# Optimization experiments

Hardware: AMD Instinct MI355X
Metric: run time of the kernel (lower is better)

Reference implementation:

```python
import jax, jax.numpy as jnp
import numpy as np

B, L, H, E, M = 8, 1024, 1024, 2048, 2048  # batch, seq, hidden_dim, expanded_dim, max_seq_length


def setup_inputs() -> dict:
    key = jax.random.key(0)
    ks = jax.random.split(key, 10)
    n = lambda k, shape, s=0.02: jax.random.normal(k, shape, jnp.float32) * s
    return {
        'x': jax.random.normal(ks[0], (B, L, H), jnp.float32),
        'ln1_w': jnp.ones((H,), jnp.float32), 'ln1_b': jnp.zeros((H,), jnp.float32),
        'ln2_w': jnp.ones((E,), jnp.float32), 'ln2_b': jnp.zeros((E,), jnp.float32),
        'w_qkv': n(ks[1], (3 * E, H)), 'b_qkv': jnp.zeros((3 * E,), jnp.float32),
        'w_out': n(ks[2], (H, E)), 'b_out': jnp.zeros((H,), jnp.float32),
        'rel_pos': n(ks[3], (2 * M - 1, H)),
        'w_beta': n(ks[4], (E, 2 * H)), 'b_beta': jnp.zeros((E,), jnp.float32),
        'w1': n(ks[5], (4 * H, H)), 'b1': jnp.zeros((4 * H,), jnp.float32),
        'w2': n(ks[6], (H, 4 * H)), 'b2': jnp.zeros((H,), jnp.float32),
        'conv_w': n(ks[7], (E, 1, 3), 0.3),  # depthwise conv1d weight [C,1,K]
        'attn_scale': jnp.ones((1,), jnp.float32),
    }


def _ln(x, w, b):
    m = jnp.mean(x, -1, keepdims=True)
    v = jnp.mean((x - m) ** 2, -1, keepdims=True)
    return (x - m) / jnp.sqrt(v + 1e-5) * w + b


def _normalize(x):
    # F.normalize(x, dim=-1): x / max(||x||_2, 1e-12)
    return x / jnp.maximum(jnp.linalg.norm(x, axis=-1, keepdims=True), 1e-12)


def _dwconv(z, w):
    # z: [B,L,E]; depthwise conv1d k=3, pad=1, no bias (groups=E)
    y = jax.lax.conv_general_dilated(
        z.transpose(0, 2, 1), w, window_strides=(1,), padding=((1, 1),),
        feature_group_count=w.shape[0], dimension_numbers=('NCH', 'OIH', 'NCH'))
    return y.transpose(0, 2, 1)


def reference(x, ln1_w, ln1_b, ln2_w, ln2_b, w_qkv, b_qkv, w_out, b_out,
              rel_pos, w_beta, b_beta, w1, b1, w2, b2, conv_w, attn_scale):
    Lx = x.shape[1]
    h = _ln(x, ln1_w, ln1_b)
    qkv = h @ w_qkv.T + b_qkv
    q, k, v = jnp.split(qkv, 3, axis=-1)  # each [B,L,E]
    q = jax.nn.silu(q)
    k = jax.nn.silu(k)
    v = jax.nn.gelu(v, approximate=False)
    # interdependent normalize-mix (k uses the updated q)
    q = _normalize(q) + 0.1 * k
    k = _normalize(k) + 0.1 * q
    q = _dwconv(q, conv_w)
    k = _dwconv(k, conv_w)
    v = _dwconv(v, conv_w)
    # position-conditioned beta gate
    pos_embed = rel_pos[:Lx]  # [L,H]
    pos_info = jnp.einsum('blh,mh->blm', h, pos_embed).mean(-1, keepdims=True)  # [B,L,1]
    comb = jnp.concatenate([h, jnp.broadcast_to(pos_info, h.shape)], axis=-1)  # [B,L,2H]
    beta = jax.nn.sigmoid(comb @ w_beta.T + b_beta) * 0.9 + 0.1  # [B,L,E]
    # delta-rule: state starts at zeros so v_old = state @ k^T = 0 exactly
    v_new = beta * v  # beta*v + (1-beta)*0
    state = jnp.einsum('ble,blf->bef', v_new, k)  # v_new^T @ k : [B,E,E]
    out = jnp.einsum('ble,bfe->blf', q, state) * attn_scale  # q @ state^T
    out = _ln(out, ln2_w, ln2_b) @ w_out.T + b_out
    x = x + out
    h2 = _ln(x, ln1_w, ln1_b)  # norm1 is reused pre-MLP
    mlp = jax.nn.gelu(h2 @ w1.T + b1, approximate=False) @ w2.T + b2
    return x + mlp
```

## Files before the change

kernel.cpp:

```cpp
#include <hip/hip_runtime.h>
#include <hip/hip_bf16.h>
#include <math.h>

using bf16 = __hip_bfloat16;
typedef __attribute__((ext_vector_type(8))) short bf16x8;
typedef __attribute__((ext_vector_type(4))) float f32x4;

#define DEVI __device__ __forceinline__

DEVI float b2f(bf16 v) { return __bfloat162float(v); }
DEVI bf16 f2b(float v) { return __float2bfloat16(v); }
DEVI float geluf(float x) { return 0.5f * x * (1.0f + erff(x * 0.70710678118654752f)); }
DEVI float siluf(float x) { return x / (1.0f + expf(-x)); }

DEVI void load_lds16(const bf16* g, bf16* l) {
  __builtin_amdgcn_global_load_lds(
      (const __attribute__((address_space(1))) void*)g,
      (__attribute__((address_space(3))) void*)l, 16, 0, 0);
}

__global__ __launch_bounds__(256) void cast_kernel(const float* __restrict__ in,
                                                   bf16* __restrict__ out, int n4) {
  int i = blockIdx.x * 256 + threadIdx.x;
  if (i >= n4) return;
  float4 v = reinterpret_cast<const float4*>(in)[i];
  bf16 o[4] = { f2b(v.x), f2b(v.y), f2b(v.z), f2b(v.w) };
  reinterpret_cast<uint2*>(out)[i] = *reinterpret_cast<uint2*>(o);
}

__global__ __launch_bounds__(256) void prep_kernel(const float* __restrict__ rel,
                                                   float* __restrict__ pm,
                                                   const float* __restrict__ wb,
                                                   float* __restrict__ wb2s) {
  const int b = blockIdx.x;
  if (b < 4) {
    int h = b * 256 + threadIdx.x;
    float s = 0.f;
    for (int m = 0; m < 1024; ++m) s += rel[m * 1024 + h];
    pm[h] = s * (1.0f / 1024.0f);
  } else {
    int e = (b - 4) * 4 + (threadIdx.x >> 6);
    int lane = threadIdx.x & 63;
    float s = 0.f;
    for (int j = lane; j < 1024; j += 64) s += wb[(long)e * 2048 + 1024 + j];
#pragma unroll
    for (int off = 32; off > 0; off >>= 1) s += __shfl_down(s, off);
    if (lane == 0) wb2s[e] = s;
  }
}

__global__ __launch_bounds__(256) void convw_pack_kernel(const float* __restrict__ cw,
                                                         bf16* __restrict__ wpl) {
  int e = blockIdx.x * 256 + threadIdx.x;
  wpl[e]        = f2b(cw[e * 3]);
  wpl[2048 + e] = f2b(cw[e * 3 + 1]);
  wpl[4096 + e] = f2b(cw[e * 3 + 2]);
}

template<bool POS>
__global__ __launch_bounds__(256) void ln1024_kernel(
    const float* __restrict__ x, const float* __restrict__ w, const float* __restrict__ b,
    bf16* __restrict__ out, const float* __restrict__ pmean, float* __restrict__ pos) {
  __shared__ float red[12];
  long row = blockIdx.x;
  int t = threadIdx.x, lane = t & 63, wid = t >> 6;
  float4 xv = reinterpret_cast<const float4*>(x + row * 1024)[t];
  float s = xv.x + xv.y + xv.z + xv.w;
  float ss = xv.x * xv.x + xv.y * xv.y + xv.z * xv.z + xv.w * xv.w;
#pragma unroll
  for (int off = 32; off > 0; off >>= 1) { s += __shfl_down(s, off); ss += __shfl_down(ss, off); }
  if (lane == 0) { red[wid] = s; red[4 + wid] = ss; }
  __syncthreads();
  s = red[0] + red[1] + red[2] + red[3];
  ss = red[4] + red[5] + red[6] + red[7];
  float mean = s * (1.0f / 1024.0f);
  float rstd = rsqrtf(ss * (1.0f / 1024.0f) - mean * mean + 1e-5f);
  float4 wv = reinterpret_cast<const float4*>(w)[t];
  float4 bv = reinterpret_cast<const float4*>(b)[t];
  float h0 = (xv.x - mean) * rstd * wv.x + bv.x;
  float h1 = (xv.y - mean) * rstd * wv.y + bv.y;
  float h2 = (xv.z - mean) * rstd * wv.z + bv.z;
  float h3 = (xv.w - mean) * rstd * wv.w + bv.w;
  bf16 o[4] = { f2b(h0), f2b(h1), f2b(h2), f2b(h3) };
  reinterpret_cast<uint2*>(out + row * 1024)[t] = *reinterpret_cast<uint2*>(o);
  if (POS) {
    float4 pv = reinterpret_cast<const float4*>(pmean)[t];
    float d = h0 * pv.x + h1 * pv.y + h2 * pv.z + h3 * pv.w;
#pragma unroll
    for (int off = 32; off > 0; off >>= 1) d += __shfl_down(d, off);
    if (lane == 0) red[8 + wid] = d;
    __syncthreads();
    if (t == 0) pos[row] = red[8] + red[9] + red[10] + red[11];
  }
}

__global__ __launch_bounds__(256) void ln1024b_kernel(
    const bf16* __restrict__ x, const float* __restrict__ w, const float* __restrict__ b,
    bf16* __restrict__ out) {
  __shared__ float red[8];
  long row = blockIdx.x;
  int t = threadIdx.x, lane = t & 63, wid = t >> 6;
  bf16 tv[4];
  *reinterpret_cast<uint2*>(tv) = reinterpret_cast<const uint2*>(x + row * 1024)[t];
  float v[4], s = 0.f, ss = 0.f;
#pragma unroll
  for (int j = 0; j < 4; ++j) { v[j] = b2f(tv[j]); s += v[j]; ss += v[j] * v[j]; }
#pragma unroll
  for (int off = 32; off > 0; off >>= 1) { s += __shfl_down(s, off); ss += __shfl_down(ss, off); }
  if (lane == 0) { red[wid] = s; red[4 + wid] = ss; }
  __syncthreads();
  s = red[0] + red[1] + red[2] + red[3];
  ss = red[4] + red[5] + red[6] + red[7];
  float mean = s * (1.0f / 1024.0f);
  float rstd = rsqrtf(ss * (1.0f / 1024.0f) - mean * mean + 1e-5f);
  float4 wv = reinterpret_cast<const float4*>(w)[t];
  float4 bv = reinterpret_cast<const float4*>(b)[t];
  bf16 o[4];
  o[0] = f2b((v[0] - mean) * rstd * wv.x + bv.x);
  o[1] = f2b((v[1] - mean) * rstd * wv.y + bv.y);
  o[2] = f2b((v[2] - mean) * rstd * wv.z + bv.z);
  o[3] = f2b((v[3] - mean) * rstd * wv.w + bv.w);
  reinterpret_cast<uint2*>(out + row * 1024)[t] = *reinterpret_cast<uint2*>(o);
}

__global__ __launch_bounds__(256) void ln2048_bf16_kernel(
    const bf16* __restrict__ in, const float* __restrict__ w, const float* __restrict__ b,
    bf16* __restrict__ out) {
  __shared__ float red[8];
  long row = blockIdx.x;
  int t = threadIdx.x, lane = t & 63, wid = t >> 6;
  bf16 tv[8];
  *reinterpret_cast<int4*>(tv) = reinterpret_cast<const int4*>(in + row * 2048)[t];
  float v[8], s = 0.f, ss = 0.f;
#pragma unroll
  for (int j = 0; j < 8; ++j) { v[j] = b2f(tv[j]); s += v[j]; ss += v[j] * v[j]; }
#pragma unroll
  for (int off = 32; off > 0; off >>= 1) { s += __shfl_down(s, off); ss += __shfl_down(ss, off); }
  if (lane == 0) { red[wid] = s; red[4 + wid] = ss; }
  __syncthreads();
  s = red[0] + red[1] + red[2] + red[3];
  ss = red[4] + red[5] + red[6] + red[7];
  float mean = s * (1.0f / 2048.0f);
  float rstd = rsqrtf(ss * (1.0f / 2048.0f) - mean * mean + 1e-5f);
  int base = t * 8;
  bf16 o[8];
#pragma unroll
  for (int j = 0; j < 8; ++j) o[j] = f2b((v[j] - mean) * rstd * w[base + j] + b[base + j]);
  reinterpret_cast<int4*>(out + row * 2048)[t] = *reinterpret_cast<int4*>(o);
}

__global__ __launch_bounds__(256) void act_norm_kernel(
    bf16* __restrict__ qp, bf16* __restrict__ kp, bf16* __restrict__ vp) {
  __shared__ float red[8];
  long row = blockIdx.x;
  int t = threadIdx.x, lane = t & 63, wid = t >> 6;
  long ob = row * 2048 + t * 8;
  bf16 tq[8], tk[8], tv[8];
  *reinterpret_cast<int4*>(tq) = *reinterpret_cast<const int4*>(qp + ob);
  *reinterpret_cast<int4*>(tk) = *reinterpret_cast<const int4*>(kp + ob);
  *reinterpret_cast<int4*>(tv) = *reinterpret_cast<const int4*>(vp + ob);
  float qs[8], ks[8];
  float sq = 0.f, sk = 0.f;
#pragma unroll
  for (int j = 0; j < 8; ++j) {
    float q = b2f(tq[j]); qs[j] = siluf(q); sq += qs[j] * qs[j];
    float k = b2f(tk[j]); ks[j] = siluf(k); sk += ks[j] * ks[j];
  }
#pragma unroll
  for (int off = 32; off > 0; off >>= 1) { sq += __shfl_down(sq, off); sk += __shfl_down(sk, off); }
  if (lane == 0) { red[wid] = sq; red[4 + wid] = sk; }
  __syncthreads();
  sq = red[0] + red[1] + red[2] + red[3];
  sk = red[4] + red[5] + red[6] + red[7];
  float rq = 1.0f / fmaxf(sqrtf(sq), 1e-12f);
  float rk = 1.0f / fmaxf(sqrtf(sk), 1e-12f);
  bf16 oq[8], ok[8], ov[8];
#pragma unroll
  for (int j = 0; j < 8; ++j) {
    float qn = qs[j] * rq + 0.1f * ks[j];
    float kn = ks[j] * rk + 0.1f * qn;
    oq[j] = f2b(qn); ok[j] = f2b(kn);
    ov[j] = f2b(geluf(b2f(tv[j])));
  }
  *reinterpret_cast<int4*>(qp + ob) = *reinterpret_cast<int4*>(oq);
  *reinterpret_cast<int4*>(kp + ob) = *reinterpret_cast<int4*>(ok);
  *reinterpret_cast<int4*>(vp + ob) = *reinterpret_cast<int4*>(ov);
}

__global__ __launch_bounds__(256) void dwconv2_kernel(
    const bf16* __restrict__ q_in, bf16* __restrict__ q_out,
    const bf16* __restrict__ v_in, bf16* __restrict__ v_out,
    const bf16* __restrict__ wpl) {
  const bf16* in = blockIdx.y ? v_in : q_in;
  bf16* out = blockIdx.y ? v_out : q_out;
  const int t = threadIdx.x;
  const int e0 = t * 8;
  const long bl = blockIdx.x;
  const int l = (int)(bl & 1023);
  const bf16* mid = in + (bl * 2048 + e0);
  bf16 tm[8], tp[8], tn[8], w0[8], w1[8], w2[8];
  *reinterpret_cast<int4*>(tm) = *reinterpret_cast<const int4*>(mid);
  if (l > 0)    *reinterpret_cast<int4*>(tp) = *reinterpret_cast<const int4*>(mid - 2048);
  if (l < 1023) *reinterpret_cast<int4*>(tn) = *reinterpret_cast<const int4*>(mid + 2048);
  *reinterpret_cast<int4*>(w0) = *reinterpret_cast<const int4*>(&wpl[e0]);
  *reinterpret_cast<int4*>(w1) = *reinterpret_cast<const int4*>(&wpl[2048 + e0]);
  *reinterpret_cast<int4*>(w2) = *reinterpret_cast<const int4*>(&wpl[4096 + e0]);
  bf16 o[8];
#pragma unroll
  for (int j = 0; j < 8; ++j) {
    float a = b2f(w1[j]) * b2f(tm[j]);
    if (l > 0) a += b2f(w0[j]) * b2f(tp[j]);
    if (l < 1023) a += b2f(w2[j]) * b2f(tn[j]);
    o[j] = f2b(a);
  }
  *reinterpret_cast<int4*>(out + (bl * 2048 + e0)) = *reinterpret_cast<int4*>(o);
}

__global__ __launch_bounds__(256) void transpose2f_kernel(
    const bf16* __restrict__ in1, bf16* __restrict__ out1,
    const bf16* __restrict__ in2, bf16* __restrict__ out2,
    const bf16* __restrict__ wpl) {
  const int zz = blockIdx.z;
  const bool isk = (zz < 8);
  const bf16* in = isk ? in1 : in2;
  bf16* out = isk ? out1 : out2;
  const long base = (long)(zz & 7) * 2097152;
  const int r0 = blockIdx.y * 64 + ((threadIdx.x & 63) >> 3) * 8;
  const int c0 = blockIdx.x * 256 + (threadIdx.x >> 6) * 64 + (threadIdx.x & 7) * 8;
  bf16 vv[8][8];
  if (isk) {
    bf16 raw[10][8];
#pragma unroll
    for (int j = 0; j < 10; ++j) {
      int r = r0 + j - 1;
      if (r >= 0 && r < 1024)
        *reinterpret_cast<int4*>(raw[j]) =
            *reinterpret_cast<const int4*>(&in[base + (long)r * 2048 + c0]);
      else {
#pragma unroll
        for (int i = 0; i < 8; ++i) raw[j][i] = f2b(0.f);
      }
    }
    bf16 w0[8], w1[8], w2[8];
    *reinterpret_cast<int4*>(w0) = *reinterpret_cast<const int4*>(&wpl[c0]);
    *reinterpret_cast<int4*>(w1) = *reinterpret_cast<const int4*>(&wpl[2048 + c0]);
    *reinterpret_cast<int4*>(w2) = *reinterpret_cast<const int4*>(&wpl[4096 + c0]);
#pragma unroll
    for (int j = 0; j < 8; ++j)
#pragma unroll
      for (int i = 0; i < 8; ++i)
        vv[j][i] = f2b(b2f(w0[i]) * b2f(raw[j][i]) + b2f(w1[i]) * b2f(raw[j + 1][i]) +
                       b2f(w2[i]) * b2f(raw[j + 2][i]));
  } else {
#pragma unroll
    for (int j = 0; j < 8; ++j)
      *reinterpret_cast<int4*>(vv[j]) =
          *reinterpret_cast<const int4*>(&in[base + (long)(r0 + j) * 2048 + c0]);
  }
#pragma unroll
  for (int i = 0; i < 8; ++i) {
    bf16 w[8];
#pragma unroll
    for (int j = 0; j < 8; ++j) w[j] = vv[j][i];
    *reinterpret_cast<int4*>(&out[base + (long)(c0 + i) * 1024 + r0]) =
        *reinterpret_cast<int4*>(w);
  }
}

enum { EPI_QKV = 0, EPI_BETA = 1, EPI_BF16 = 2, EPI_SCALE = 3, EPI_RES_F32 = 4, EPI_GELU = 5 };

#define MF(d, a, b) d = __builtin_amdgcn_mfma_f32_16x16x32_bf16(a, b, d, 0, 0, 0)
#define RD_A(S, MR, KK) \
  (*reinterpret_cast<const bf16x8*>(&smem[(S)*16384 + wm*8192 + ((MR)*16 + r16)*64 + ((((KK)*32) + kq8) ^ swz)]))
#define RD_B(S, NR, KK) \
  (*reinterpret_cast<const bf16x8*>(&smem[32768 + (S)*16384 + (wn>>1)*8192 + ((wn&1)*64 + (NR)*16 + r16)*64 + ((((KK)*32) + kq8) ^ swz)]))
#define STAGE_A1(S, H, Q, KT) \
  load_lds16(Abase + (long)((H)*128 + (Q)*64) * lda + (long)(KT)*64, \
             &smem[(S)*16384 + (H)*8192 + (Q)*4096 + wid*512])
#define STAGE_B1(S, H, Q, KT) \
  load_lds16(Bbase + (long)((H)*128 + (Q)*64) * ldb + (long)(KT)*64, \
             &smem[32768 + (S)*16384 + (H)*8192 + (Q)*4096 + wid*512])
#define STAGE_AH(S, H, KT) { STAGE_A1(S, H, 0, KT); STAGE_A1(S, H, 1, KT); }
#define STAGE_BH(S, H, KT) { STAGE_B1(S, H, 0, KT); STAGE_B1(S, H, 1, KT); }
#define BAR_A __builtin_amdgcn_s_barrier()
#define LGKM0 { asm volatile("s_waitcnt lgkmcnt(0)" ::: "memory"); __builtin_amdgcn_sched_barrier(0); }
#define VWAIT(LST) { if (LST) { asm volatile("s_waitcnt vmcnt(0)" ::: "memory"); } \
                     else     { asm volatile("s_waitcnt vmcnt(6)" ::: "memory"); } \
                     __builtin_amdgcn_sched_barrier(0); }

#define KTILE(S, ST1, ST2, ST3, ST4, W4) { \
  bf16x8 aL[4][2], aH[4][2], bL[2][2], bH[2][2]; \
  _Pragma("unroll") for (int m_ = 0; m_ < 4; ++m_) { aL[m_][0] = RD_A(S, m_, 0); aL[m_][1] = RD_A(S, m_, 1); } \
  _Pragma("unroll") for (int n_ = 0; n_ < 2; ++n_) { bL[n_][0] = RD_B(S, n_, 0); bL[n_][1] = RD_B(S, n_, 1); } \
  ST1; BAR_A; LGKM0; \
  __builtin_amdgcn_s_setprio(1); \
  _Pragma("unroll") for (int m_ = 0; m_ < 4; ++m_) _Pragma("unroll") for (int n_ = 0; n_ < 2; ++n_) { \
    MF(acc[m_][n_], aL[m_][0], bL[n_][0]); MF(acc[m_][n_], aL[m_][1], bL[n_][1]); } \
  __builtin_amdgcn_s_setprio(0); __builtin_amdgcn_s_barrier(); \
  _Pragma("unroll") for (int n_ = 0; n_ < 2; ++n_) { bH[n_][0] = RD_B(S, n_ + 2, 0); bH[n_][1] = RD_B(S, n_ + 2, 1); } \
  ST2; BAR_A; LGKM0; \
  __builtin_amdgcn_s_setprio(1); \
  _Pragma("unroll") for (int m_ = 0; m_ < 4; ++m_) _Pragma("unroll") for (int n_ = 0; n_ < 2; ++n_) { \
    MF(acc[m_][n_ + 2], aL[m_][0], bH[n_][0]); MF(acc[m_][n_ + 2], aL[m_][1], bH[n_][1]); } \
  __builtin_amdgcn_s_setprio(0); __builtin_amdgcn_s_barrier(); \
  _Pragma("unroll") for (int m_ = 0; m_ < 4; ++m_) { aH[m_][0] = RD_A(S, m_ + 4, 0); aH[m_][1] = RD_A(S, m_ + 4, 1); } \
  ST3; BAR_A; LGKM0; \
  __builtin_amdgcn_s_setprio(1); \
  _Pragma("unroll") for (int m_ = 0; m_ < 4; ++m_) _Pragma("unroll") for (int n_ = 0; n_ < 2; ++n_) { \
    MF(acc[m_ + 4][n_], aH[m_][0], bL[n_][0]); MF(acc[m_ + 4][n_], aH[m_][1], bL[n_][1]); } \
  __builtin_amdgcn_s_setprio(0); __builtin_amdgcn_s_barrier(); \
  ST4; W4; BAR_A; LGKM0; \
  __builtin_amdgcn_s_setprio(1); \
  _Pragma("unroll") for (int m_ = 0; m_ < 4; ++m_) _Pragma("unroll") for (int n_ = 0; n_ < 2; ++n_) { \
    MF(acc[m_ + 4][n_ + 2], aH[m_][0], bH[n_][0]); MF(acc[m_ + 4][n_ + 2], aH[m_][1], bH[n_][1]); } \
  __builtin_amdgcn_s_setprio(0); __builtin_amdgcn_s_barrier(); \
}

template<int EPI>
__global__ __launch_bounds__(512) void gemm256_kernel(
    const bf16* __restrict__ A, int lda, long sA,
    const bf16* __restrict__ B, int ldb, long sB,
    void* __restrict__ Cv, int ldc, long sC, int K,
    const float* __restrict__ bias, const float* __restrict__ aux_row,
    const float* __restrict__ aux_col, const bf16* __restrict__ vconv,
    const float* __restrict__ resid, const float* __restrict__ scale_ptr,
    bf16* __restrict__ p2, bf16* __restrict__ p3) {
  __shared__ bf16 smem[65536];
  const int bz = blockIdx.z;
  A += (long)bz * sA;
  B += (long)bz * sB;
  const int m0 = blockIdx.y * 256, n0 = blockIdx.x * 256;
  const int t = threadIdx.x, lane = t & 63, wid = t >> 6;
  const int wm = wid >> 2, wn = wid & 3;
  const int r16 = lane & 15, kq8 = (lane >> 4) * 8;
  const int swz = (r16 & 7) << 3;
  const int lrow = lane >> 3;
  const int cswz = ((lane & 7) ^ lrow) * 8;
  const bf16* Abase = A + (long)(m0 + wid * 8 + lrow) * lda + cswz;
  const bf16* Bbase = B + (long)(n0 + wid * 8 + lrow) * ldb + cswz;
  f32x4 acc[8][4] = {};
  const int NT = K >> 6, NIT = NT >> 1;
  STAGE_AH(0, 0, 0); STAGE_AH(0, 1, 0); STAGE_BH(0, 0, 0); STAGE_BH(0, 1, 0);
  STAGE_BH(1, 0, 1); STAGE_BH(1, 1, 1); STAGE_AH(1, 0, 1);
  asm volatile("s_waitcnt vmcnt(6)" ::: "memory");
  __builtin_amdgcn_sched_barrier(0);
  __builtin_amdgcn_s_barrier();
  for (int i = 0; i < NIT; ++i) {
    const int tb = 2 * i;
    const bool lst = (i == NIT - 1);
    KTILE(0,
      { STAGE_AH(1, 1, tb + 1); },
      { },
      { if (!lst) { STAGE_BH(0, 0, tb + 2); STAGE_BH(0, 1, tb + 2); } },
      { if (!lst) { STAGE_AH(0, 0, tb + 2); } },
      VWAIT(lst));
    KTILE(1,
      { if (!lst) { STAGE_AH(0, 1, tb + 2); } },
      { },
      { if (!lst) { STAGE_BH(1, 0, tb + 3); STAGE_BH(1, 1, tb + 3); } },
      { if (!lst) { STAGE_AH(1, 0, tb + 3); } },
      VWAIT(lst));
  }
  float scl = 1.0f;
  if (EPI == EPI_SCALE) scl = scale_ptr[0];
  const int rb = (lane >> 4) * 4;
#pragma unroll
  for (int mr = 0; mr < 8; ++mr) {
#pragma unroll
    for (int nr = 0; nr < 4; ++nr) {
#pragma unroll
      for (int r = 0; r < 4; ++r) {
        const long gm = m0 + wm * 128 + mr * 16 + rb + r;
        const int gn = n0 + wn * 64 + nr * 16 + r16;
        const long idx = (long)bz * sC + gm * (long)ldc + gn;
        float v = acc[mr][nr][r];
        if (EPI == EPI_QKV) {
          const int seg = gn >> 11, cc = gn & 2047;
          bf16* dst = (seg == 0) ? (bf16*)Cv : (seg == 1) ? p2 : p3;
          dst[gm * 2048 + cc] = f2b(v + bias[gn]);
        } else if (EPI == EPI_BETA) {
          float tt = v + bias[gn] + aux_row[gm] * aux_col[gn];
          float be = 0.9f / (1.0f + expf(-tt)) + 0.1f;
          ((bf16*)Cv)[idx] = f2b(be * b2f(vconv[idx]));
        } else if (EPI == EPI_BF16) {
          ((bf16*)Cv)[idx] = f2b(v);
        } else if (EPI == EPI_SCALE) {
          ((bf16*)Cv)[idx] = f2b(v * scl);
        } else if (EPI == EPI_RES_F32) {
          ((float*)Cv)[idx] = v + bias[gn] + resid[idx];
        } else {
          ((bf16*)Cv)[idx] = f2b(geluf(v + bias[gn]));
        }
      }
    }
  }
}

#define A_RD(S, MR, KK) \
  (*reinterpret_cast<const bf16x8*>(&amem[(S)*8192 + (wm*64 + (MR)*16 + r16)*64 + ((((KK)*32) + kq8) ^ swz)]))
#define B_RD(S, NR, KK) \
  (*reinterpret_cast<const bf16x8*>(&amem[16384 + (S)*16384 + (wn*64 + (NR)*16 + r16)*64 + ((((KK)*32) + kq8) ^ swz)]))
#define A_ST(S, Q, KT) \
  load_lds16(Abase + (long)((Q)*64) * lda + (long)(KT)*64, &amem[(S)*8192 + (Q)*4096 + wid*512])
#define B_ST(S, Q, KT) \
  load_lds16(Bbase + (long)((Q)*64) * ldb + (long)(KT)*64, &amem[16384 + (S)*16384 + (Q)*4096 + wid*512])
#define STAGE_T(S, KT) { A_ST(S, 0, KT); A_ST(S, 1, KT); B_ST(S, 0, KT); B_ST(S, 1, KT); B_ST(S, 2, KT); B_ST(S, 3, KT); }

template<int RB, int WB>
__global__ __launch_bounds__(512) void gemmA128_kernel(
    const bf16* __restrict__ A, int lda,
    const bf16* __restrict__ B, int ldb,
    void* __restrict__ Cv, int ldc, int K,
    const float* __restrict__ bias, const void* __restrict__ residv) {
  __shared__ bf16 amem[49152];
  const int m0 = blockIdx.y * 128, n0 = blockIdx.x * 256;
  const int t = threadIdx.x, lane = t & 63, wid = t >> 6;
  const int wm = wid >> 2, wn = wid & 3;
  const int r16 = lane & 15, kq8 = (lane >> 4) * 8;
  const int swz = (r16 & 7) << 3;
  const int lrow = lane >> 3;
  const int cswz = ((lane & 7) ^ lrow) * 8;
  const bf16* Abase = A + (long)(m0 + wid * 8 + lrow) * lda + cswz;
  const bf16* Bbase = B + (long)(n0 + wid * 8 + lrow) * ldb + cswz;
  f32x4 acc[4][4] = {};
  const int NT = K >> 6;
  STAGE_T(0, 0); STAGE_T(1, 1);
  asm volatile("s_waitcnt vmcnt(6)" ::: "memory");
  __builtin_amdgcn_sched_barrier(0);
  __builtin_amdgcn_s_barrier();
  for (int tt = 0; tt < NT; ++tt) {
    const int S = tt & 1;
    const bool pre = (tt + 2 < NT);
    bf16x8 a[4][2], bL[2][2], bH[2][2];
#pragma unroll
    for (int m_ = 0; m_ < 4; ++m_) { a[m_][0] = A_RD(S, m_, 0); a[m_][1] = A_RD(S, m_, 1); }
#pragma unroll
    for (int n_ = 0; n_ < 2; ++n_) { bL[n_][0] = B_RD(S, n_, 0); bL[n_][1] = B_RD(S, n_, 1); }
#pragma unroll
    for (int n_ = 0; n_ < 2; ++n_) { bH[n_][0] = B_RD(S, n_ + 2, 0); bH[n_][1] = B_RD(S, n_ + 2, 1); }
    LGKM0;
    __builtin_amdgcn_s_setprio(1);
#pragma unroll
    for (int m_ = 0; m_ < 4; ++m_)
#pragma unroll
      for (int n_ = 0; n_ < 2; ++n_) {
        MF(acc[m_][n_], a[m_][0], bL[n_][0]); MF(acc[m_][n_], a[m_][1], bL[n_][1]);
      }
    __builtin_amdgcn_s_setprio(0);
    __builtin_amdgcn_s_barrier();
    __builtin_amdgcn_sched_barrier(0);
    if (pre) STAGE_T(S, tt + 2);
    __builtin_amdgcn_s_setprio(1);
#pragma unroll
    for (int m_ = 0; m_ < 4; ++m_)
#pragma unroll
      for (int n_ = 0; n_ < 2; ++n_) {
        MF(acc[m_][n_ + 2], a[m_][0], bH[n_][0]); MF(acc[m_][n_ + 2], a[m_][1], bH[n_][1]);
      }
    __builtin_amdgcn_s_setprio(0);
    if (pre) { asm volatile("s_waitcnt vmcnt(6)" ::: "memory"); }
    else     { asm volatile("s_waitcnt vmcnt(0)" ::: "memory"); }
    __builtin_amdgcn_sched_barrier(0);
    __builtin_amdgcn_s_barrier();
    __builtin_amdgcn_sched_barrier(0);
  }
  const int rb = (lane >> 4) * 4;
#pragma unroll
  for (int mr = 0; mr < 4; ++mr) {
#pragma unroll
    for (int nr = 0; nr < 4; ++nr) {
#pragma unroll
      for (int r = 0; r < 4; ++r) {
        const long gm = m0 + wm * 64 + mr * 16 + rb + r;
        const int gn = n0 + wn * 64 + nr * 16 + r16;
        const long idx = gm * (long)ldc + gn;
        float rv = RB ? b2f(((const bf16*)residv)[idx]) : ((const float*)residv)[idx];
        float o = acc[mr][nr][r] + bias[gn] + rv;
        if (WB) ((bf16*)Cv)[idx] = f2b(o);
        else    ((float*)Cv)[idx] = o;
      }
    }
  }
}

extern "C" void kernel_launch(void* const* d_in, const int* in_sizes, int n_in,
                              void* d_out, int out_size, void* d_ws, size_t ws_size,
                              hipStream_t stream) {
  (void)in_sizes; (void)n_in; (void)out_size;
  const float* x       = (const float*)d_in[0];
  const float* ln1_w   = (const float*)d_in[1];
  const float* ln1_b   = (const float*)d_in[2];
  const float* ln2_w   = (const float*)d_in[3];
  const float* ln2_b   = (const float*)d_in[4];
  const float* w_qkv   = (const float*)d_in[5];
  const float* b_qkv   = (const float*)d_in[6];
  const float* w_out   = (const float*)d_in[7];
  const float* b_out   = (const float*)d_in[8];
  const float* rel_pos = (const float*)d_in[9];
  const float* w_beta  = (const float*)d_in[10];
  const float* b_beta  = (const float*)d_in[11];
  const float* w1      = (const float*)d_in[12];
  const float* b1      = (const float*)d_in[13];
  const float* w2      = (const float*)d_in[14];
  const float* b2      = (const float*)d_in[15];
  const float* conv_w  = (const float*)d_in[16];
  const float* attn_sc = (const float*)d_in[17];
  float* out = (float*)d_out;

  if (ws_size < 180400128UL) return;
  char* ws = (char*)d_ws;
  bf16*  wbuf    = (bf16*)(ws + 0);
  bf16*  wpl     = (bf16*)(ws + 11534336UL);
  float* pmean   = (float*)(ws + 12582912UL);
  float* wb2s    = (float*)(ws + 12587008UL);
  float* posinfo = (float*)(ws + 12595200UL);
  bf16* R0 = (bf16*)(ws + 12627968UL);
  bf16* R1 = (bf16*)(ws + 46182400UL);
  bf16* R2 = (bf16*)(ws + 79736832UL);
  bf16* R3 = (bf16*)(ws + 113291264UL);
  bf16* R4 = (bf16*)(ws + 146845696UL);
  bf16* vscr = (bf16*)d_out;
  bf16* x2b = R1;

  prep_kernel<<<516, 256, 0, stream>>>(rel_pos, pmean, w_beta, wb2s);

  ln1024_kernel<true><<<8192, 256, 0, stream>>>(x, ln1_w, ln1_b, R0, pmean, posinfo);

  cast_kernel<<<6144, 256, 0, stream>>>(w_qkv, wbuf, 1572864);
  gemm256_kernel<EPI_QKV><<<dim3(24, 32, 1), 512, 0, stream>>>(
      R0, 1024, 0, wbuf, 1024, 0, R1, 2048, 0, 1024,
      b_qkv, nullptr, nullptr, nullptr, nullptr, nullptr, R2, R3);

  act_norm_kernel<<<8192, 256, 0, stream>>>(R1, R2, R3);

  convw_pack_kernel<<<8, 256, 0, stream>>>(conv_w, wpl);
  dwconv2_kernel<<<dim3(8192, 2), 256, 0, stream>>>(R1, R4, R3, vscr, wpl);

  cast_kernel<<<4096, 256, 0, stream>>>(w_beta, wbuf, 1048576);
  gemm256_kernel<EPI_BETA><<<dim3(8, 32, 1), 512, 0, stream>>>(
      R0, 1024, 0, wbuf, 2048, 0, R1, 2048, 0, 1024,
      b_beta, posinfo, wb2s, vscr, nullptr, nullptr, nullptr, nullptr);

  transpose2f_kernel<<<dim3(8, 16, 16), 256, 0, stream>>>(R2, R3, R1, R0, wpl);

  gemm256_kernel<EPI_BF16><<<dim3(8, 8, 8), 512, 0, stream>>>(
      R0, 1024, 2097152, R3, 1024, 2097152, R1, 2048, 4194304, 1024,
      nullptr, nullptr, nullptr, nullptr, nullptr, nullptr, nullptr, nullptr);

  gemm256_kernel<EPI_SCALE><<<dim3(8, 4, 8), 512, 0, stream>>>(
      R4, 2048, 2097152, R1, 2048, 4194304, R3, 2048, 2097152, 2048,
      nullptr, nullptr, nullptr, nullptr, nullptr, attn_sc, nullptr, nullptr);

  ln2048_bf16_kernel<<<8192, 256, 0, stream>>>(R3, ln2_w, ln2_b, R0);

  cast_kernel<<<2048, 256, 0, stream>>>(w_out, wbuf, 524288);
  gemmA128_kernel<0, 1><<<dim3(4, 64, 1), 512, 0, stream>>>(
      R0, 2048, wbuf, 2048, x2b, 1024, 2048, b_out, x);

  ln1024b_kernel<<<8192, 256, 0, stream>>>(x2b, ln1_w, ln1_b, R2);

  cast_kernel<<<4096, 256, 0, stream>>>(w1, wbuf, 1048576);
  gemm256_kernel<EPI_GELU><<<dim3(16, 32, 1), 512, 0, stream>>>(
      R2, 1024, 0, wbuf, 1024, 0, R3, 4096, 0, 1024,
      b1, nullptr, nullptr, nullptr, nullptr, nullptr, nullptr, nullptr);

  cast_kernel<<<4096, 256, 0, stream>>>(w2, wbuf, 1048576);
  gemmA128_kernel<1, 0><<<dim3(4, 64, 1), 512, 0, stream>>>(
      R3, 4096, wbuf, 4096, out, 1024, 4096, b2, x2b);
}
```

Before: 732.9 us.

## Reassociate linear attention as (q k^T) v to halve matmul flops

Computes q·k^T (an LxL matrix) first and then multiplies by the transposed v_new, instead of forming the ExE state v^T k and multiplying q by it. Because there is no causal mask the result is mathematically the same, and the flop count drops since L is smaller than E. The k convolution now runs through the separate dwconv kernel, and only v is transposed. gemmA128 gains a batched, epilogue-free variant for the q·k^T step. Rounding the LxL intermediate to bf16 changes the rounding behaviour.

```diff
diff --git a/kernel.cpp b/kernel.cpp
--- a/kernel.cpp
+++ b/kernel.cpp
@@ -188,11 +188,11 @@
 }
 
 __global__ __launch_bounds__(256) void dwconv2_kernel(
-    const bf16* __restrict__ q_in, bf16* __restrict__ q_out,
-    const bf16* __restrict__ v_in, bf16* __restrict__ v_out,
+    const bf16* __restrict__ a_in, bf16* __restrict__ a_out,
+    const bf16* __restrict__ b_in, bf16* __restrict__ b_out,
     const bf16* __restrict__ wpl) {
-  const bf16* in = blockIdx.y ? v_in : q_in;
-  bf16* out = blockIdx.y ? v_out : q_out;
+  const bf16* in = blockIdx.y ? b_in : a_in;
+  bf16* out = blockIdx.y ? b_out : a_out;
   const int t = threadIdx.x;
   const int e0 = t * 8;
   const long bl = blockIdx.x;
@@ -216,52 +216,21 @@
   *reinterpret_cast<int4*>(out + (bl * 2048 + e0)) = *reinterpret_cast<int4*>(o);
 }
 
-__global__ __launch_bounds__(256) void transpose2f_kernel(
-    const bf16* __restrict__ in1, bf16* __restrict__ out1,
-    const bf16* __restrict__ in2, bf16* __restrict__ out2,
-    const bf16* __restrict__ wpl) {
-  const int zz = blockIdx.z;
-  const bool isk = (zz < 8);
-  const bf16* in = isk ? in1 : in2;
-  bf16* out = isk ? out1 : out2;
-  const long base = (long)(zz & 7) * 2097152;
+__global__ __launch_bounds__(256) void transpose_kernel(const bf16* __restrict__ in,
+                                                        bf16* __restrict__ out) {
+  const long base = (long)blockIdx.z * 2097152;
   const int r0 = blockIdx.y * 64 + ((threadIdx.x & 63) >> 3) * 8;
   const int c0 = blockIdx.x * 256 + (threadIdx.x >> 6) * 64 + (threadIdx.x & 7) * 8;
-  bf16 vv[8][8];
-  if (isk) {
-    bf16 raw[10][8];
-#pragma unroll
-    for (int j = 0; j < 10; ++j) {
-      int r = r0 + j - 1;
-      if (r >= 0 && r < 1024)
-        *reinterpret_cast<int4*>(raw[j]) =
-            *reinterpret_cast<const int4*>(&in[base + (long)r * 2048 + c0]);
-      else {
-#pragma unroll
-        for (int i = 0; i < 8; ++i) raw[j][i] = f2b(0.f);
-      }
-    }
-    bf16 w0[8], w1[8], w2[8];
-    *reinterpret_cast<int4*>(w0) = *reinterpret_cast<const int4*>(&wpl[c0]);
-    *reinterpret_cast<int4*>(w1) = *reinterpret_cast<const int4*>(&wpl[2048 + c0]);
-    *reinterpret_cast<int4*>(w2) = *reinterpret_cast<const int4*>(&wpl[4096 + c0]);
-#pragma unroll
-    for (int j = 0; j < 8; ++j)
-#pragma unroll
-      for (int i = 0; i < 8; ++i)
-        vv[j][i] = f2b(b2f(w0[i]) * b2f(raw[j][i]) + b2f(w1[i]) * b2f(raw[j + 1][i]) +
-                       b2f(w2[i]) * b2f(raw[j + 2][i]));
-  } else {
-#pragma unroll
-    for (int j = 0; j < 8; ++j)
-      *reinterpret_cast<int4*>(vv[j]) =
-          *reinterpret_cast<const int4*>(&in[base + (long)(r0 + j) * 2048 + c0]);
-  }
+  bf16 v[8][8];
+#pragma unroll
+  for (int j = 0; j < 8; ++j)
+    *reinterpret_cast<int4*>(v[j]) =
+        *reinterpret_cast<const int4*>(&in[base + (long)(r0 + j) * 2048 + c0]);
 #pragma unroll
   for (int i = 0; i < 8; ++i) {
     bf16 w[8];
 #pragma unroll
-    for (int j = 0; j < 8; ++j) w[j] = vv[j][i];
+    for (int j = 0; j < 8; ++j) w[j] = v[j][i];
     *reinterpret_cast<int4*>(&out[base + (long)(c0 + i) * 1024 + r0]) =
         *reinterpret_cast<int4*>(w);
   }
@@ -406,13 +375,15 @@
   load_lds16(Bbase + (long)((Q)*64) * ldb + (long)(KT)*64, &amem[16384 + (S)*16384 + (Q)*4096 + wid*512])
 #define STAGE_T(S, KT) { A_ST(S, 0, KT); A_ST(S, 1, KT); B_ST(S, 0, KT); B_ST(S, 1, KT); B_ST(S, 2, KT); B_ST(S, 3, KT); }
 
-template<int RB, int WB>
+template<int RB, int WB, int NR>
 __global__ __launch_bounds__(512) void gemmA128_kernel(
-    const bf16* __restrict__ A, int lda,
-    const bf16* __restrict__ B, int ldb,
-    void* __restrict__ Cv, int ldc, int K,
+    const bf16* __restrict__ A, int lda, long sA,
+    const bf16* __restrict__ B, int ldb, long sB,
+    void* __restrict__ Cv, int ldc, long sC, int K,
     const float* __restrict__ bias, const void* __restrict__ residv) {
   __shared__ bf16 amem[49152];
+  A += (long)blockIdx.z * sA;
+  B += (long)blockIdx.z * sB;
   const int m0 = blockIdx.y * 128, n0 = blockIdx.x * 256;
   const int t = threadIdx.x, lane = t & 63, wid = t >> 6;
   const int wm = wid >> 2, wn = wid & 3;
@@ -473,9 +444,12 @@
       for (int r = 0; r < 4; ++r) {
         const long gm = m0 + wm * 64 + mr * 16 + rb + r;
         const int gn = n0 + wn * 64 + nr * 16 + r16;
-        const long idx = gm * (long)ldc + gn;
-        float rv = RB ? b2f(((const bf16*)residv)[idx]) : ((const float*)residv)[idx];
-        float o = acc[mr][nr][r] + bias[gn] + rv;
+        const long idx = (long)blockIdx.z * sC + gm * (long)ldc + gn;
+        float o = acc[mr][nr][r];
+        if (!NR) {
+          o += bias[gn];
+          o += RB ? b2f(((const bf16*)residv)[idx]) : ((const float*)residv)[idx];
+        }
         if (WB) ((bf16*)Cv)[idx] = f2b(o);
         else    ((float*)Cv)[idx] = o;
       }
@@ -541,21 +515,23 @@
       R0, 1024, 0, wbuf, 2048, 0, R1, 2048, 0, 1024,
       b_beta, posinfo, wb2s, vscr, nullptr, nullptr, nullptr, nullptr);
 
-  transpose2f_kernel<<<dim3(8, 16, 16), 256, 0, stream>>>(R2, R3, R1, R0, wpl);
-
-  gemm256_kernel<EPI_BF16><<<dim3(8, 8, 8), 512, 0, stream>>>(
-      R0, 1024, 2097152, R3, 1024, 2097152, R1, 2048, 4194304, 1024,
-      nullptr, nullptr, nullptr, nullptr, nullptr, nullptr, nullptr, nullptr);
+  dwconv2_kernel<<<dim3(8192, 1), 256, 0, stream>>>(R2, R3, R2, R3, wpl);
+
+  transpose_kernel<<<dim3(8, 16, 8), 256, 0, stream>>>(R1, R0);
+
+  gemmA128_kernel<0, 1, 1><<<dim3(4, 8, 8), 512, 0, stream>>>(
+      R4, 2048, 2097152, R3, 2048, 2097152, R2, 1024, 1048576, 2048,
+      nullptr, nullptr);
 
   gemm256_kernel<EPI_SCALE><<<dim3(8, 4, 8), 512, 0, stream>>>(
-      R4, 2048, 2097152, R1, 2048, 4194304, R3, 2048, 2097152, 2048,
+      R2, 1024, 1048576, R0, 1024, 2097152, R3, 2048, 2097152, 1024,
       nullptr, nullptr, nullptr, nullptr, nullptr, attn_sc, nullptr, nullptr);
 
   ln2048_bf16_kernel<<<8192, 256, 0, stream>>>(R3, ln2_w, ln2_b, R0);
 
   cast_kernel<<<2048, 256, 0, stream>>>(w_out, wbuf, 524288);
-  gemmA128_kernel<0, 1><<<dim3(4, 64, 1), 512, 0, stream>>>(
-      R0, 2048, wbuf, 2048, x2b, 1024, 2048, b_out, x);
+  gemmA128_kernel<0, 1, 0><<<dim3(4, 64, 1), 512, 0, stream>>>(
+      R0, 2048, 0, wbuf, 2048, 0, x2b, 1024, 0, 2048, b_out, x);
 
   ln1024b_kernel<<<8192, 256, 0, stream>>>(x2b, ln1_w, ln1_b, R2);
 
@@ -565,6 +541,6 @@
       b1, nullptr, nullptr, nullptr, nullptr, nullptr, nullptr, nullptr);
 
   cast_kernel<<<4096, 256, 0, stream>>>(w2, wbuf, 1048576);
-  gemmA128_kernel<1, 0><<<dim3(4, 64, 1), 512, 0, stream>>>(
-      R3, 4096, wbuf, 4096, out, 1024, 4096, b2, x2b);
-}
+  gemmA128_kernel<1, 0, 0><<<dim3(4, 64, 1), 512, 0, stream>>>(
+      R3, 4096, 0, wbuf, 4096, 0, out, 1024, 0, 4096, b2, x2b);
+}
```

New measurement: 685.8 us. 1.07x faster.
